# Performance work log

Measured on AMD Instinct MI355X. Metric: run time of the kernel, lower is better.

The kernel has to match this reference:

```python
import jax, jax.numpy as jnp
import numpy as np

H = 256  # hidden size of nn.RNN(1, 256)


def setup_inputs() -> dict:
    key = jax.random.key(0)
    k1, k2, k3, k4, k5 = jax.random.split(key, 5)
    B, T = 4096, 256
    bound = 1.0 / np.sqrt(H)  # PyTorch RNN default init: U(-1/sqrt(H), 1/sqrt(H))
    return {
        "T": T,
        "flat_img": jax.random.normal(k1, (B, T), dtype=jnp.float32),
        "W_ih": jax.random.uniform(k2, (H, 1), minval=-bound, maxval=bound, dtype=jnp.float32),
        "W_hh": jax.random.uniform(k3, (H, H), minval=-bound, maxval=bound, dtype=jnp.float32),
        "b_ih": jax.random.uniform(k4, (H,), minval=-bound, maxval=bound, dtype=jnp.float32),
        "b_hh": jax.random.uniform(k5, (H,), minval=-bound, maxval=bound, dtype=jnp.float32),
    }


def reference(T, flat_img, W_ih, W_hh, b_ih, b_hh):
    B = flat_img.shape[0]
    dtype = flat_img.dtype
    latent0 = jnp.zeros((1, B, H), dtype)

    # timestep = arange(T, 0, -1); t_prime = T - t runs 0..T-1 in loop order
    ts = jnp.arange(T, 0, -1).astype(dtype)
    a_t = (ts + 1.0) / (T + 1.0)
    sigmas = jnp.sqrt(a_t * (1.0 - a_t))          # [T]
    xs = flat_img[:, :T].T                         # [T, B], row i is flat_img[:, t_prime=i]
    noise_keys = jax.random.split(jax.random.key(42), T)

    w_ih = W_ih[:, 0]                              # input_size == 1 -> matvec is a broadcast

    def step(latent, inp):
        x_t, sigma_t, k = inp
        x = x_t[None, :, None]                     # [1, B, 1]
        # single RNN-tanh step: tanh(x W_ih^T + b_ih + h W_hh^T + b_hh)
        h = jnp.tanh(x * w_ih + b_ih + jnp.einsum('lbh,gh->lbg', latent, W_hh) + b_hh)
        eps = 0.1 * jax.random.normal(k, latent.shape, dtype)
        latent = latent + x + h + sigma_t * eps    # x broadcasts [1,B,1]->[1,B,H]
        return latent, None

    latent, _ = jax.lax.scan(step, latent0, (xs, sigmas, noise_keys))
    return latent
```

## Files before the change

kernel.cpp:

```cpp
#include <hip/hip_runtime.h>


#define TSTEPS 256
#define HDIM   256
#define ROWS   16
#define LSTR   264
#define TILE   (ROWS * LSTR)
#define XSTR   260

typedef _Float16 half8 __attribute__((ext_vector_type(8)));
typedef __attribute__((ext_vector_type(4))) float float4v;

struct U2 { unsigned x, y; };

__device__ __forceinline__ void tfround(unsigned &x0, unsigned &x1, const int r) {
  x0 += x1;
  x1 = __builtin_rotateleft32(x1, r);
  x1 ^= x0;
}

__device__ __forceinline__ U2 threefry(unsigned k0, unsigned k1, unsigned x0, unsigned x1) {
  unsigned k2 = k0 ^ k1 ^ 0x1BD11BDAu;
  x0 += k0; x1 += k1;
  tfround(x0,x1,13); tfround(x0,x1,15); tfround(x0,x1,26); tfround(x0,x1,6);
  x0 += k1; x1 += k2 + 1u;
  tfround(x0,x1,17); tfround(x0,x1,29); tfround(x0,x1,16); tfround(x0,x1,24);
  x0 += k2; x1 += k0 + 2u;
  tfround(x0,x1,13); tfround(x0,x1,15); tfround(x0,x1,26); tfround(x0,x1,6);
  x0 += k0; x1 += k1 + 3u;
  tfround(x0,x1,17); tfround(x0,x1,29); tfround(x0,x1,16); tfround(x0,x1,24);
  x0 += k1; x1 += k2 + 4u;
  tfround(x0,x1,13); tfround(x0,x1,15); tfround(x0,x1,26); tfround(x0,x1,6);
  x0 += k2; x1 += k0 + 5u;
  return {x0, x1};
}

__device__ __forceinline__ float jax_normal_from_bits(unsigned bits) {
#pragma clang fp contract(off)
  const float LO = __builtin_bit_cast(float, 0xBF7FFFFFu);
  float f = __builtin_bit_cast(float, (bits >> 9) | 0x3f800000u) - 1.0f;
  float u = fmaf(f, 2.0f, LO);
  u = fmaxf(u, LO);
  float t1 = u * u;
  float s  = 1.0f - t1;
  float w  = -0.6931471805599453f * __builtin_amdgcn_logf(s);
  float p;
  if (w < 5.0f) {
    float z = w - 2.5f;
    p = 2.81022636e-08f;
    p = fmaf(p, z, 3.43273939e-07f);
    p = fmaf(p, z, -3.5233877e-06f);
    p = fmaf(p, z, -4.39150654e-06f);
    p = fmaf(p, z, 0.00021858087f);
    p = fmaf(p, z, -0.00125372503f);
    p = fmaf(p, z, -0.00417768164f);
    p = fmaf(p, z, 0.246640727f);
    p = fmaf(p, z, 1.50140941f);
  } else {
    float z = sqrtf(w) - 3.0f;
    p = -0.000200214257f;
    p = fmaf(p, z, 0.000100950558f);
    p = fmaf(p, z, 0.00134934322f);
    p = fmaf(p, z, -0.00367342844f);
    p = fmaf(p, z, 0.00573950773f);
    p = fmaf(p, z, -0.0076224613f);
    p = fmaf(p, z, 0.00943887047f);
    p = fmaf(p, z, 1.00167406f);
    p = fmaf(p, z, 2.83297682f);
  }
  return 1.4142135623730951f * (p * u);
}

__device__ __forceinline__ float4v mfma_f16(half8 a, half8 b, float4v c) {
  return __builtin_amdgcn_mfma_f32_16x16x32_f16(a, b, c, 0, 0, 0);
}

__global__ __launch_bounds__(1024, 4)
void drnet_kernel(const float* __restrict__ flat_img,
                  const float* __restrict__ W_ih,
                  const float* __restrict__ W_hh,
                  const float* __restrict__ b_ih,
                  const float* __restrict__ b_hh,
                  float* __restrict__ out)
{
  __shared__ __align__(16) char lds_pool[86016];
  float*    x_sh    = (float*)lds_pool;
  unsigned* keys_sh = (unsigned*)(lds_pool + 16640);
  short*    latp    = (short*)(lds_pool + 18688);

  const int tid  = threadIdx.x;
  const int wg   = blockIdx.x;
  const int wv   = tid >> 6;
  const int lane = tid & 63;
  const int q    = lane >> 4;
  const int c    = lane & 15;

  if (tid < TSTEPS) {
    U2 kk = threefry(0u, 42u, 0u, (unsigned)tid);
    keys_sh[2*tid]   = kk.x;
    keys_sh[2*tid+1] = kk.y;
  }

  {
    int i = tid * 4;
    int m = i >> 8;
    float4v v = *(const float4v*)(flat_img + (size_t)wg * (ROWS*TSTEPS) + i);
    *(float4v*)&x_sh[m * XSTR + (i & 255)] = v;
  }

  {
    int* p0 = (int*)latp;
    for (int i = tid; i < 2 * TILE; i += 1024) p0[i] = 0;
  }

  half8 Wh[8], Wl[8];
  const int g = wv*16 + c;
  const float bias = b_ih[g] + b_hh[g];
  const float wih  = W_ih[g];
  #pragma unroll
  for (int kk = 0; kk < 8; ++kk) {
    const float* wp = W_hh + g*HDIM + kk*32 + q*8;
    float4v w0 = *(const float4v*)wp;
    float4v w1 = *(const float4v*)(wp + 4);
    half8 h8, l8;
    #pragma unroll
    for (int j2 = 0; j2 < 4; ++j2) {
      float f0 = w0[j2], f1 = w1[j2];
      _Float16 h0 = (_Float16)f0, h1 = (_Float16)f1;
      _Float16 l0 = (_Float16)((f0 - (float)h0) * 2048.0f);
      _Float16 l1 = (_Float16)((f1 - (float)h1) * 2048.0f);
      h8[j2] = h0; h8[j2+4] = h1;
      l8[j2] = l0; l8[j2+4] = l1;
    }
    Wh[kk] = h8; Wl[kk] = l8;
  }

  float lat[4] = {0.f, 0.f, 0.f, 0.f};

  const unsigned jbase = ((unsigned)(wg*ROWS + q*4) << 8) + (unsigned)g;
  const int aoff = c * LSTR + q * 8;
  const int woff = (q*4) * LSTR + wv*16 + c;

  __syncthreads();

  for (int t = 0; t < TSTEPS; ++t) {
    unsigned kA = (unsigned)__builtin_amdgcn_readfirstlane((int)keys_sh[2*t]);
    unsigned kB = (unsigned)__builtin_amdgcn_readfirstlane((int)keys_sh[2*t+1]);

    float tsf = (float)(TSTEPS - t);
    float a_t = (tsf + 1.0f) / 257.0f;
    float escale = 0.1f * sqrtf(a_t * (1.0f - a_t));

    const short* rb = latp + (t & 1) * (2*TILE) + aoff;
    short*       wb = latp + ((t + 1) & 1) * (2*TILE) + woff;

    float4v aa = {0.f, 0.f, 0.f, 0.f};
    float4v ab = {0.f, 0.f, 0.f, 0.f};
    #pragma unroll
    for (int kk = 0; kk < 8; ++kk) {
      half8 ah = *(const half8*)(rb + 0*TILE + kk*32);
      half8 al = *(const half8*)(rb + 1*TILE + kk*32);
      aa = mfma_f16(ah, Wh[kk], aa);
      ab = mfma_f16(al, Wh[kk], ab);
      ab = mfma_f16(ah, Wl[kk], ab);
      if (kk < 4) {
        unsigned j = jbase + (unsigned)(kk << 8);
        U2 rr = threefry(kA, kB, 0u, j);
        float nrm = jax_normal_from_bits(rr.x ^ rr.y);
        lat[kk] = fmaf(escale, nrm, lat[kk]);
      }
    }

    float xr[4];
    #pragma unroll
    for (int r = 0; r < 4; ++r) xr[r] = x_sh[(q*4 + r) * XSTR + t];

    #pragma unroll
    for (int r = 0; r < 4; ++r) {
      float d = aa[r] + ab[r] * (1.0f / 2048.0f);
      float pre = d + fmaf(xr[r], wih, bias);
      float h;
      if (__builtin_fabsf(pre) >= 7.90531110763549805f) {
        h = pre > 0.0f ? 1.0f : -1.0f;
      } else {
        float e = __builtin_amdgcn_exp2f(pre * 2.8853900817779268f);
        h = fmaf(-2.0f, __builtin_amdgcn_rcpf(e + 1.0f), 1.0f);
      }
      float nl = lat[r] + xr[r] + h;
      lat[r] = nl;
      _Float16 hh = (_Float16)nl;
      _Float16 ll = (_Float16)((nl - (float)hh) * 2048.0f);
      short* wp = wb + r*LSTR;
      wp[0]    = __builtin_bit_cast(short, hh);
      wp[TILE] = __builtin_bit_cast(short, ll);
    }
    __syncthreads();
  }

  #pragma unroll
  for (int r = 0; r < 4; ++r)
    out[jbase + (unsigned)(r << 8)] = lat[r];
}

extern "C" void kernel_launch(void* const* d_in, const int* in_sizes, int n_in,
                              void* d_out, int out_size, void* d_ws, size_t ws_size,
                              hipStream_t stream) {
  (void)in_sizes; (void)n_in; (void)out_size; (void)d_ws; (void)ws_size;
  const float* flat_img = (const float*)d_in[1];
  const float* W_ih     = (const float*)d_in[2];
  const float* W_hh     = (const float*)d_in[3];
  const float* b_ih     = (const float*)d_in[4];
  const float* b_hh     = (const float*)d_in[5];
  drnet_kernel<<<dim3(4096 / ROWS), dim3(1024), 0, stream>>>(
      flat_img, W_ih, W_hh, b_ih, b_hh, (float*)d_out);
}
```

Baseline: 987.7 us.

## Precompute noise in a separate fully parallel kernel and stream it into the scan

Adds a kernel that generates all B*T*H Gaussian noise values with threefry into a 1 GiB workspace, laid out to match the scan's per-lane access. The scan kernel then prefetches one float4 of noise per step instead of running threefry and the inverse-erf inside the serial recurrence. This takes RNG work off the critical path and gives it full GPU parallelism, at the cost of writing and reading 1 GiB of global memory. If the workspace is too small, the original fused kernel runs instead.

Result: no change. 989.4 us (+0.2%).

```diff
diff --git a/kernel.cpp b/kernel.cpp
--- a/kernel.cpp
+++ b/kernel.cpp
@@ -75,18 +75,42 @@
   return __builtin_amdgcn_mfma_f32_16x16x32_f16(a, b, c, 0, 0, 0);
 }
 
+__global__ __launch_bounds__(256, 8)
+void drnet_rng(float* __restrict__ nws) {
+  const unsigned bid = blockIdx.x;
+  const unsigned t   = bid >> 6;
+  U2 kk = threefry(0u, 42u, 0u, t);
+  unsigned kA = (unsigned)__builtin_amdgcn_readfirstlane((int)kk.x);
+  unsigned kB = (unsigned)__builtin_amdgcn_readfirstlane((int)kk.y);
+  const unsigned base = bid * 16384u + threadIdx.x * 4u;
+  #pragma unroll 4
+  for (unsigned s = 0; s < 16; ++s) {
+    unsigned e0 = base + (s << 10);
+    unsigned b0 = ((e0 >> 12) & 255u) * 16u + ((e0 >> 6) & 3u) * 4u;
+    unsigned g  = ((e0 >> 8) & 15u) * 16u + ((e0 >> 2) & 15u);
+    unsigned j0 = b0 * 256u + g;
+    float4v v;
+    #pragma unroll
+    for (int r = 0; r < 4; ++r) {
+      U2 rr = threefry(kA, kB, 0u, j0 + ((unsigned)r << 8));
+      v[r] = jax_normal_from_bits(rr.x ^ rr.y);
+    }
+    *(float4v*)(nws + e0) = v;
+  }
+}
+
 __global__ __launch_bounds__(1024, 4)
-void drnet_kernel(const float* __restrict__ flat_img,
-                  const float* __restrict__ W_ih,
-                  const float* __restrict__ W_hh,
-                  const float* __restrict__ b_ih,
-                  const float* __restrict__ b_hh,
-                  float* __restrict__ out)
+void drnet_scan(const float* __restrict__ flat_img,
+                const float* __restrict__ W_ih,
+                const float* __restrict__ W_hh,
+                const float* __restrict__ b_ih,
+                const float* __restrict__ b_hh,
+                const float* __restrict__ nws,
+                float* __restrict__ out)
 {
   __shared__ __align__(16) char lds_pool[86016];
-  float*    x_sh    = (float*)lds_pool;
-  unsigned* keys_sh = (unsigned*)(lds_pool + 16640);
-  short*    latp    = (short*)(lds_pool + 18688);
+  float* x_sh = (float*)lds_pool;
+  short* latp = (short*)(lds_pool + 16640);
 
   const int tid  = threadIdx.x;
   const int wg   = blockIdx.x;
@@ -95,19 +119,12 @@
   const int q    = lane >> 4;
   const int c    = lane & 15;
 
-  if (tid < TSTEPS) {
-    U2 kk = threefry(0u, 42u, 0u, (unsigned)tid);
-    keys_sh[2*tid]   = kk.x;
-    keys_sh[2*tid+1] = kk.y;
-  }
-
   {
     int i = tid * 4;
     int m = i >> 8;
     float4v v = *(const float4v*)(flat_img + (size_t)wg * (ROWS*TSTEPS) + i);
     *(float4v*)&x_sh[m * XSTR + (i & 255)] = v;
   }
-
   {
     int* p0 = (int*)latp;
     for (int i = tid; i < 2 * TILE; i += 1024) p0[i] = 0;
@@ -136,16 +153,21 @@
   }
 
   float lat[4] = {0.f, 0.f, 0.f, 0.f};
-
   const unsigned jbase = ((unsigned)(wg*ROWS + q*4) << 8) + (unsigned)g;
   const int aoff = c * LSTR + q * 8;
   const int woff = (q*4) * LSTR + wv*16 + c;
 
+  const float4v* np = (const float4v*)nws + ((unsigned)wg*1024u + (unsigned)wv*64u + (unsigned)lane);
+  float4v nz_pend = np[0];
+
   __syncthreads();
 
   for (int t = 0; t < TSTEPS; ++t) {
-    unsigned kA = (unsigned)__builtin_amdgcn_readfirstlane((int)keys_sh[2*t]);
-    unsigned kB = (unsigned)__builtin_amdgcn_readfirstlane((int)keys_sh[2*t+1]);
+    float4v nz = nz_pend;
+    {
+      int tn = t + 1 < TSTEPS ? t + 1 : t;
+      nz_pend = np[(size_t)tn * 262144u];
+    }
 
     float tsf = (float)(TSTEPS - t);
     float a_t = (tsf + 1.0f) / 257.0f;
@@ -163,13 +185,10 @@
       aa = mfma_f16(ah, Wh[kk], aa);
       ab = mfma_f16(al, Wh[kk], ab);
       ab = mfma_f16(ah, Wl[kk], ab);
-      if (kk < 4) {
-        unsigned j = jbase + (unsigned)(kk << 8);
-        U2 rr = threefry(kA, kB, 0u, j);
-        float nrm = jax_normal_from_bits(rr.x ^ rr.y);
-        lat[kk] = fmaf(escale, nrm, lat[kk]);
-      }
-    }
+    }
+
+    #pragma unroll
+    for (int r = 0; r < 4; ++r) lat[r] = fmaf(escale, nz[r], lat[r]);
 
     float xr[4];
     #pragma unroll
@@ -202,15 +221,146 @@
     out[jbase + (unsigned)(r << 8)] = lat[r];
 }
 
+__global__ __launch_bounds__(1024, 4)
+void drnet_fused(const float* __restrict__ flat_img,
+                 const float* __restrict__ W_ih,
+                 const float* __restrict__ W_hh,
+                 const float* __restrict__ b_ih,
+                 const float* __restrict__ b_hh,
+                 float* __restrict__ out)
+{
+  __shared__ __align__(16) char lds_pool[86016];
+  float*    x_sh    = (float*)lds_pool;
+  unsigned* keys_sh = (unsigned*)(lds_pool + 16640);
+  short*    latp    = (short*)(lds_pool + 18688);
+
+  const int tid  = threadIdx.x;
+  const int wg   = blockIdx.x;
+  const int wv   = tid >> 6;
+  const int lane = tid & 63;
+  const int q    = lane >> 4;
+  const int c    = lane & 15;
+
+  if (tid < TSTEPS) {
+    U2 kk = threefry(0u, 42u, 0u, (unsigned)tid);
+    keys_sh[2*tid]   = kk.x;
+    keys_sh[2*tid+1] = kk.y;
+  }
+  {
+    int i = tid * 4;
+    int m = i >> 8;
+    float4v v = *(const float4v*)(flat_img + (size_t)wg * (ROWS*TSTEPS) + i);
+    *(float4v*)&x_sh[m * XSTR + (i & 255)] = v;
+  }
+  {
+    int* p0 = (int*)latp;
+    for (int i = tid; i < 2 * TILE; i += 1024) p0[i] = 0;
+  }
+
+  half8 Wh[8], Wl[8];
+  const int g = wv*16 + c;
+  const float bias = b_ih[g] + b_hh[g];
+  const float wih  = W_ih[g];
+  #pragma unroll
+  for (int kk = 0; kk < 8; ++kk) {
+    const float* wp = W_hh + g*HDIM + kk*32 + q*8;
+    float4v w0 = *(const float4v*)wp;
+    float4v w1 = *(const float4v*)(wp + 4);
+    half8 h8, l8;
+    #pragma unroll
+    for (int j2 = 0; j2 < 4; ++j2) {
+      float f0 = w0[j2], f1 = w1[j2];
+      _Float16 h0 = (_Float16)f0, h1 = (_Float16)f1;
+      _Float16 l0 = (_Float16)((f0 - (float)h0) * 2048.0f);
+      _Float16 l1 = (_Float16)((f1 - (float)h1) * 2048.0f);
+      h8[j2] = h0; h8[j2+4] = h1;
+      l8[j2] = l0; l8[j2+4] = l1;
+    }
+    Wh[kk] = h8; Wl[kk] = l8;
+  }
+
+  float lat[4] = {0.f, 0.f, 0.f, 0.f};
+  const unsigned jbase = ((unsigned)(wg*ROWS + q*4) << 8) + (unsigned)g;
+  const int aoff = c * LSTR + q * 8;
+  const int woff = (q*4) * LSTR + wv*16 + c;
+
+  __syncthreads();
+
+  for (int t = 0; t < TSTEPS; ++t) {
+    unsigned kA = (unsigned)__builtin_amdgcn_readfirstlane((int)keys_sh[2*t]);
+    unsigned kB = (unsigned)__builtin_amdgcn_readfirstlane((int)keys_sh[2*t+1]);
+
+    float tsf = (float)(TSTEPS - t);
+    float a_t = (tsf + 1.0f) / 257.0f;
+    float escale = 0.1f * sqrtf(a_t * (1.0f - a_t));
+
+    const short* rb = latp + (t & 1) * (2*TILE) + aoff;
+    short*       wb = latp + ((t + 1) & 1) * (2*TILE) + woff;
+
+    float4v aa = {0.f, 0.f, 0.f, 0.f};
+    float4v ab = {0.f, 0.f, 0.f, 0.f};
+    #pragma unroll
+    for (int kk = 0; kk < 8; ++kk) {
+      half8 ah = *(const half8*)(rb + 0*TILE + kk*32);
+      half8 al = *(const half8*)(rb + 1*TILE + kk*32);
+      aa = mfma_f16(ah, Wh[kk], aa);
+      ab = mfma_f16(al, Wh[kk], ab);
+      ab = mfma_f16(ah, Wl[kk], ab);
+      if (kk < 4) {
+        unsigned j = jbase + (unsigned)(kk << 8);
+        U2 rr = threefry(kA, kB, 0u, j);
+        float nrm = jax_normal_from_bits(rr.x ^ rr.y);
+        lat[kk] = fmaf(escale, nrm, lat[kk]);
+      }
+    }
+
+    float xr[4];
+    #pragma unroll
+    for (int r = 0; r < 4; ++r) xr[r] = x_sh[(q*4 + r) * XSTR + t];
+
+    #pragma unroll
+    for (int r = 0; r < 4; ++r) {
+      float d = aa[r] + ab[r] * (1.0f / 2048.0f);
+      float pre = d + fmaf(xr[r], wih, bias);
+      float h;
+      if (__builtin_fabsf(pre) >= 7.90531110763549805f) {
+        h = pre > 0.0f ? 1.0f : -1.0f;
+      } else {
+        float e = __builtin_amdgcn_exp2f(pre * 2.8853900817779268f);
+        h = fmaf(-2.0f, __builtin_amdgcn_rcpf(e + 1.0f), 1.0f);
+      }
+      float nl = lat[r] + xr[r] + h;
+      lat[r] = nl;
+      _Float16 hh = (_Float16)nl;
+      _Float16 ll = (_Float16)((nl - (float)hh) * 2048.0f);
+      short* wp = wb + r*LSTR;
+      wp[0]    = __builtin_bit_cast(short, hh);
+      wp[TILE] = __builtin_bit_cast(short, ll);
+    }
+    __syncthreads();
+  }
+
+  #pragma unroll
+  for (int r = 0; r < 4; ++r)
+    out[jbase + (unsigned)(r << 8)] = lat[r];
+}
+
 extern "C" void kernel_launch(void* const* d_in, const int* in_sizes, int n_in,
                               void* d_out, int out_size, void* d_ws, size_t ws_size,
                               hipStream_t stream) {
-  (void)in_sizes; (void)n_in; (void)out_size; (void)d_ws; (void)ws_size;
+  (void)in_sizes; (void)n_in; (void)out_size;
   const float* flat_img = (const float*)d_in[1];
   const float* W_ih     = (const float*)d_in[2];
   const float* W_hh     = (const float*)d_in[3];
   const float* b_ih     = (const float*)d_in[4];
   const float* b_hh     = (const float*)d_in[5];
-  drnet_kernel<<<dim3(4096 / ROWS), dim3(1024), 0, stream>>>(
-      flat_img, W_ih, W_hh, b_ih, b_hh, (float*)d_out);
-}
+  const size_t need = (size_t)268435456 * 4;
+  if (ws_size >= need) {
+    drnet_rng<<<dim3(16384), dim3(256), 0, stream>>>((float*)d_ws);
+    drnet_scan<<<dim3(4096 / ROWS), dim3(1024), 0, stream>>>(
+        flat_img, W_ih, W_hh, b_ih, b_hh, (const float*)d_ws, (float*)d_out);
+  } else {
+    drnet_fused<<<dim3(4096 / ROWS), dim3(1024), 0, stream>>>(
+        flat_img, W_ih, W_hh, b_ih, b_hh, (float*)d_out);
+  }
+}
```
